# Kernel optimization log

Hardware: AMD Instinct MI355X
Metric: run time of the kernel (lower is better)

## Reference

```python
import jax, jax.numpy as jnp
import numpy as np
import math

B, S, E = 2, 2048, 1024
H, D = 16, 64
LAMBDA_INIT = 0.8
GN_EPS = 1e-5


def setup_inputs() -> dict:
    key = jax.random.key(0)
    ks = jax.random.split(key, 12)
    s = 0.02
    inputs = jax.random.normal(ks[0], (B, S, E), jnp.float32)
    attention_mask = jnp.ones((B, S), jnp.float32)
    token_indices = jnp.sort(jax.random.randint(ks[1], (B, S), 0, S), axis=-1)
    Wq = jax.random.normal(ks[2], (2 * H * D, E), jnp.float32) * s
    Wk = jax.random.normal(ks[3], (2 * H * D, E), jnp.float32) * s
    Wv = jax.random.normal(ks[4], (H * D, E), jnp.float32) * s
    Wo = jax.random.normal(ks[5], (E, H * D), jnp.float32) * s
    lam_q1 = jax.random.normal(ks[6], (D,), jnp.float32) * 0.1
    lam_q2 = jax.random.normal(ks[7], (D,), jnp.float32) * 0.1
    lam_k1 = jax.random.normal(ks[8], (D,), jnp.float32) * 0.1
    lam_k2 = jax.random.normal(ks[9], (D,), jnp.float32) * 0.1
    gn_w = jnp.ones((H * D,), jnp.float32)
    gn_b = jnp.zeros((H * D,), jnp.float32)
    return dict(inputs=inputs, attention_mask=attention_mask, token_indices=token_indices,
                Wq=Wq, Wk=Wk, Wv=Wv, Wo=Wo,
                lam_q1=lam_q1, lam_q2=lam_q2, lam_k1=lam_k1, lam_k2=lam_k2,
                gn_w=gn_w, gn_b=gn_b)


def reference(inputs, attention_mask, token_indices, Wq, Wk, Wv, Wo,
              lam_q1, lam_q2, lam_k1, lam_k2, gn_w, gn_b):
    b, s, e = inputs.shape
    # projections: q,k have doubled head dim (differential), v is standard
    q = (inputs @ Wq.T).reshape(b, s, H, 2 * D).transpose(0, 2, 1, 3)  # [B,H,S,2D]
    k = (inputs @ Wk.T).reshape(b, s, H, 2 * D).transpose(0, 2, 1, 3)
    v = (inputs @ Wv.T).reshape(b, s, H, D).transpose(0, 2, 1, 3)      # [B,H,S,D]
    Q1, Q2 = q[..., :D], q[..., D:]
    K1, K2 = k[..., :D], k[..., D:]
    scale = 1.0 / math.sqrt(D)
    s1 = jnp.einsum('bhqd,bhkd->bhqk', Q1, K1) * scale
    s2 = jnp.einsum('bhqd,bhkd->bhqk', Q2, K2) * scale
    # ALiBi bias: slopes[h] * (pos_q - pos_k), subtracted
    slopes = 2.0 ** (-8.0 * jnp.arange(1, H + 1, dtype=jnp.float32) / H)
    pos = token_indices.astype(jnp.float32)                            # [B,S]
    pos_diff = pos[:, :, None] - pos[:, None, :]                       # [B,S,S]
    bias = slopes[None, :, None, None] * pos_diff[:, None, :, :]       # [B,H,S,S]
    # causal + padding masks
    causal = jnp.triu(jnp.full((s, s), -1e9, jnp.float32), 1)[None, None]
    pad = (1.0 - attention_mask)[:, None, None, :] * -1e9
    s1 = s1 - bias + causal + pad
    s2 = s2 - bias + causal + pad
    w1 = jax.nn.softmax(s1, axis=-1)
    w2 = jax.nn.softmax(s2, axis=-1)
    lam = jnp.exp(jnp.dot(lam_q1, lam_k1)) - jnp.exp(jnp.dot(lam_q2, lam_k2)) + LAMBDA_INIT
    w = w1 - lam * w2
    out = jnp.einsum('bhqk,bhkd->bhqd', w, v)                          # [B,H,S,D]
    # GroupNorm(num_groups=H, num_channels=H*D) over channels-first layout [B,C,S]
    x = out.transpose(0, 2, 1, 3).reshape(b, s, H * D).transpose(0, 2, 1)  # [B,C,S]
    xg = x.reshape(b, H, D * s)
    mean = xg.mean(axis=-1, keepdims=True)
    var = xg.var(axis=-1, keepdims=True)
    xn = ((xg - mean) / jnp.sqrt(var + GN_EPS)).reshape(b, H * D, s)
    xn = xn * gn_w[None, :, None] + gn_b[None, :, None]
    xn = xn * (1.0 - LAMBDA_INIT)
    attn = xn.transpose(0, 2, 1)                                       # [B,S,H*D]
    return attn @ Wo.T
```

## Files before the change

kernel.cpp:

```cpp
#include <hip/hip_runtime.h>
#include <hip/hip_bf16.h>

typedef __hip_bfloat16 bf16;
typedef float f32x4 __attribute__((ext_vector_type(4)));
typedef float fvec4 __attribute__((ext_vector_type(4)));
typedef short s16x8 __attribute__((ext_vector_type(8)));

#define NB_B 2
#define NB_S 2048
#define NB_E 1024
#define NB_H 16
#define NB_D 64

typedef const __attribute__((address_space(1))) void* GPTR;
typedef __attribute__((address_space(3))) void* LPTR;

__device__ __forceinline__ void gld16(const void* g, void* l) {
  __builtin_amdgcn_global_load_lds((GPTR)g, (LPTR)l, 16, 0, 0);
}

__device__ __forceinline__ s16x8 ld8(const bf16* p) { return *(const s16x8*)p; }

__device__ __forceinline__ f32x4 MFMA(s16x8 a, s16x8 b, f32x4 c) {
  return __builtin_amdgcn_mfma_f32_16x16x32_bf16(a, b, c, 0, 0, 0);
}

struct __align__(8) bf16x4 { bf16 a, b, c, d; };

__global__ void prep_kernel(const float* __restrict__ inputs,
                            const float* __restrict__ wq, const float* __restrict__ wk,
                            const float* __restrict__ wv, const float* __restrict__ wo,
                            const float* __restrict__ lq1, const float* __restrict__ lq2,
                            const float* __restrict__ lk1, const float* __restrict__ lk2,
                            bf16* __restrict__ xbf,
                            bf16* __restrict__ oq, bf16* __restrict__ ok,
                            bf16* __restrict__ ov, bf16* __restrict__ oo,
                            float* __restrict__ lamo) {
  const int blk = blockIdx.x;
  if (blk < 4096) {
    int i = blk * 256 + threadIdx.x;
    fvec4 v = ((const fvec4*)inputs)[i];
    bf16x4 o = { bf16(v.x), bf16(v.y), bf16(v.z), bf16(v.w) };
    ((bf16x4*)xbf)[i] = o;
  } else if (blk < 10240) {
    int i = (blk - 4096) * 256 + threadIdx.x;
    const float* src; bf16* dst; int off;
    if (i < 524288)       { src = wq; dst = oq; off = i; }
    else if (i < 1048576) { src = wk; dst = ok; off = i - 524288; }
    else if (i < 1310720) { src = wv; dst = ov; off = i - 1048576; }
    else                  { src = wo; dst = oo; off = i - 1310720; }
    fvec4 v = ((const fvec4*)src)[off];
    bf16x4 o = { bf16(v.x), bf16(v.y), bf16(v.z), bf16(v.w) };
    ((bf16x4*)dst)[off] = o;
  } else {
    int l = threadIdx.x;
    if (l < 64) {
      float d1 = lq1[l] * lk1[l];
      float d2 = lq2[l] * lk2[l];
#pragma unroll
      for (int o = 32; o; o >>= 1) { d1 += __shfl_xor(d1, o); d2 += __shfl_xor(d2, o); }
      if (l == 0) lamo[0] = expf(d1) - expf(d2) + 0.8f;
    }
  }
}

__global__ void combo_kernel(const int* __restrict__ tok, const float* __restrict__ amask,
                             float* __restrict__ combo) {
  int i = blockIdx.x * 256 + threadIdx.x;
  int hh = i >> 12, bs = i & 4095;
  float slopeL = exp2f(-0.5f * (float)(hh + 1)) * 1.44269504088896340736f;
  combo[i] = slopeL * (float)tok[bs] + (amask[bs] - 1.f) * 1.44269504e9f;
}

__global__ void gn_coef(const float* __restrict__ gnp, const float* __restrict__ gw,
                        const float* __restrict__ gb,
                        float* __restrict__ Sc, float* __restrict__ Tc) {
  int i = blockIdx.x * 256 + threadIdx.x;
  int b = i >> 10, c = i & 1023;
  int bh = b * 16 + (c >> 6);
  float mean = gnp[bh * 2] * (1.f / 131072.f);
  float var = gnp[bh * 2 + 1] * (1.f / 131072.f) - mean * mean;
  float rstd = rsqrtf(var + 1e-5f) * 0.2f;
  float S = rstd * gw[c];
  Sc[i] = S;
  Tc[i] = 0.2f * gb[c] - mean * S;
}

template <int EPI>
__global__ __launch_bounds__(256) void gemm_bt(const bf16* __restrict__ A,
                                               const bf16* __restrict__ Bw,
                                               bf16* __restrict__ Ob,
                                               bf16* __restrict__ Ob2,
                                               bf16* __restrict__ Ob3,
                                               float* __restrict__ Of,
                                               int Kd, float oscale) {
  __shared__ bf16 As[2][128 * 32];
  __shared__ bf16 Bs[2][128 * 32];
  const int tid = threadIdx.x;
  const int lane = tid & 63;
  const int fr = lane & 15, fq = lane >> 4;
  const int wave = tid >> 6;
  const int wr = (wave >> 1) * 64, wc = (wave & 1) * 64;
  const size_t m0 = (size_t)blockIdx.x * 128, n0 = (size_t)blockIdx.y * 128;

  f32x4 acc[4][4];
#pragma unroll
  for (int i = 0; i < 4; i++)
#pragma unroll
    for (int j = 0; j < 4; j++) acc[i][j] = f32x4{0.f, 0.f, 0.f, 0.f};

  const int ca = tid, cb = tid + 256;
  const bf16* ga0 = A + (m0 + (ca >> 2)) * Kd + (ca & 3) * 8;
  const bf16* ga1 = A + (m0 + (cb >> 2)) * Kd + (cb & 3) * 8;
  const bf16* gb0 = Bw + (n0 + (ca >> 2)) * Kd + (ca & 3) * 8;
  const bf16* gb1 = Bw + (n0 + (cb >> 2)) * Kd + (cb & 3) * 8;

  gld16(ga0, &As[0][ca * 8]);
  gld16(ga1, &As[0][cb * 8]);
  gld16(gb0, &Bs[0][ca * 8]);
  gld16(gb1, &Bs[0][cb * 8]);
  __syncthreads();

  const int NKT = Kd >> 5;
  for (int kti = 0; kti < NKT; ++kti) {
    const int cur = kti & 1;
    if (kti + 1 < NKT) {
      const int kt = (kti + 1) << 5;
      gld16(ga0 + kt, &As[cur ^ 1][ca * 8]);
      gld16(ga1 + kt, &As[cur ^ 1][cb * 8]);
      gld16(gb0 + kt, &Bs[cur ^ 1][ca * 8]);
      gld16(gb1 + kt, &Bs[cur ^ 1][cb * 8]);
    }
    s16x8 af[4], bfv[4];
#pragma unroll
    for (int mi = 0; mi < 4; mi++) af[mi] = ld8(&As[cur][(wr + mi * 16 + fr) * 32 + fq * 8]);
#pragma unroll
    for (int ni = 0; ni < 4; ni++) bfv[ni] = ld8(&Bs[cur][(wc + ni * 16 + fr) * 32 + fq * 8]);
#pragma unroll
    for (int mi = 0; mi < 4; mi++)
#pragma unroll
      for (int ni = 0; ni < 4; ni++)
        acc[mi][ni] = MFMA(af[mi], bfv[ni], acc[mi][ni]);
    __syncthreads();
  }

  bf16* dst = Ob;
  size_t nsub = 0;
  float osc = oscale;
  bool isV = false;
  if constexpr (EPI == 0) {
    if (n0 >= 4096)      { dst = Ob3; nsub = 4096; osc = 1.0f; isV = true; }
    else if (n0 >= 2048) { dst = Ob2; nsub = 2048; osc = 1.0f; }
  }

  if constexpr (EPI == 0) {
    if (isV) {
#pragma unroll
      for (int mi = 0; mi < 4; mi++)
#pragma unroll
        for (int ni = 0; ni < 4; ni++) {
          size_t m = m0 + wr + mi * 16 + fq * 4;
          size_t n = n0 + wc + ni * 16 + fr;
          size_t nn = n - 4096;
          size_t b = m >> 11, s = m & 2047, h = nn >> 6, d = nn & 63;
          bf16x4 o = { bf16(acc[mi][ni][0]), bf16(acc[mi][ni][1]),
                       bf16(acc[mi][ni][2]), bf16(acc[mi][ni][3]) };
          *(bf16x4*)&dst[((b * NB_H + h) * NB_D + d) * NB_S + s] = o;
        }
    } else {
#pragma unroll
      for (int mi = 0; mi < 4; mi++)
#pragma unroll
        for (int ni = 0; ni < 4; ni++)
#pragma unroll
          for (int i = 0; i < 4; i++) {
            size_t m = m0 + wr + mi * 16 + fq * 4 + i;
            size_t n = n0 + wc + ni * 16 + fr;
            float v = acc[mi][ni][i] * osc;
            size_t nn = n - nsub;
            size_t b = m >> 11, s = m & 2047, h = nn >> 7, dd = nn & 127;
            dst[((b * NB_H + h) * NB_S + s) * 128 + dd] = bf16(v);
          }
    }
  } else {
#pragma unroll
    for (int mi = 0; mi < 4; mi++)
#pragma unroll
      for (int ni = 0; ni < 4; ni++)
#pragma unroll
        for (int i = 0; i < 4; i++) {
          size_t m = m0 + wr + mi * 16 + fq * 4 + i;
          size_t n = n0 + wc + ni * 16 + fr;
          Of[m * 1024 + n] = acc[mi][ni][i] * oscale;
        }
  }
}

__device__ __forceinline__ s16x8 gn_chunk(const bf16* __restrict__ Xb, size_t base, int tb,
                                          int k, const float* __restrict__ Sc,
                                          const float* __restrict__ Tc) {
  s16x8 xv = *(const s16x8*)(Xb + base + (size_t)(k >> 6) * 131072 + (k & 63));
  const float* sp = Sc + tb + k;
  const float* tp = Tc + tb + k;
  fvec4 s0v = *(const fvec4*)sp, s1v = *(const fvec4*)(sp + 4);
  fvec4 t0v = *(const fvec4*)tp, t1v = *(const fvec4*)(tp + 4);
  float sv[8] = { s0v.x, s0v.y, s0v.z, s0v.w, s1v.x, s1v.y, s1v.z, s1v.w };
  float tv[8] = { t0v.x, t0v.y, t0v.z, t0v.w, t1v.x, t1v.y, t1v.z, t1v.w };
  bf16 o8[8];
#pragma unroll
  for (int j = 0; j < 8; j++) {
    const float xf = __uint_as_float(((unsigned)(unsigned short)xv[j]) << 16);
    o8[j] = bf16(xf * sv[j] + tv[j]);
  }
  return *(const s16x8*)o8;
}

__global__ __launch_bounds__(256) void gemm_out(const bf16* __restrict__ Xb,
                                                const bf16* __restrict__ Bw,
                                                const float* __restrict__ Sc,
                                                const float* __restrict__ Tc,
                                                float* __restrict__ Of) {
  __shared__ bf16 As[2][128 * 32];
  __shared__ bf16 Bs[2][128 * 32];
  const int tid = threadIdx.x;
  const int lane = tid & 63;
  const int fr = lane & 15, fq = lane >> 4;
  const int wave = tid >> 6;
  const int wr = (wave >> 1) * 64, wc = (wave & 1) * 64;
  const size_t m0 = (size_t)blockIdx.x * 128, n0 = (size_t)blockIdx.y * 128;

  f32x4 acc[4][4];
#pragma unroll
  for (int i = 0; i < 4; i++)
#pragma unroll
    for (int j = 0; j < 4; j++) acc[i][j] = f32x4{0.f, 0.f, 0.f, 0.f};

  const int ca = tid, cb = tid + 256;
  const int ma = (int)m0 + (ca >> 2), mb = (int)m0 + (cb >> 2);
  const int koa = (ca & 3) * 8, kob = (cb & 3) * 8;
  const size_t basea = (size_t)(ma >> 11) * 2097152 + (size_t)(ma & 2047) * 64;
  const size_t baseb = (size_t)(mb >> 11) * 2097152 + (size_t)(mb & 2047) * 64;
  const int tba = (ma >> 11) * 1024, tbb = (mb >> 11) * 1024;

  const bf16* gb0 = Bw + (n0 + (ca >> 2)) * 1024 + koa;
  const bf16* gb1 = Bw + (n0 + (cb >> 2)) * 1024 + kob;

  {
    s16x8 a0 = gn_chunk(Xb, basea, tba, koa, Sc, Tc);
    s16x8 a1 = gn_chunk(Xb, baseb, tbb, kob, Sc, Tc);
    gld16(gb0, &Bs[0][ca * 8]);
    gld16(gb1, &Bs[0][cb * 8]);
    *(s16x8*)&As[0][ca * 8] = a0;
    *(s16x8*)&As[0][cb * 8] = a1;
  }
  __syncthreads();

  for (int kti = 0; kti < 32; ++kti) {
    const int cur = kti & 1;
    s16x8 na0, na1;
    if (kti + 1 < 32) {
      const int kt = (kti + 1) << 5;
      na0 = gn_chunk(Xb, basea, tba, kt + koa, Sc, Tc);
      na1 = gn_chunk(Xb, baseb, tbb, kt + kob, Sc, Tc);
      gld16(gb0 + kt, &Bs[cur ^ 1][ca * 8]);
      gld16(gb1 + kt, &Bs[cur ^ 1][cb * 8]);
    }
    s16x8 af[4], bfv[4];
#pragma unroll
    for (int mi = 0; mi < 4; mi++) af[mi] = ld8(&As[cur][(wr + mi * 16 + fr) * 32 + fq * 8]);
#pragma unroll
    for (int ni = 0; ni < 4; ni++) bfv[ni] = ld8(&Bs[cur][(wc + ni * 16 + fr) * 32 + fq * 8]);
#pragma unroll
    for (int mi = 0; mi < 4; mi++)
#pragma unroll
      for (int ni = 0; ni < 4; ni++)
        acc[mi][ni] = MFMA(af[mi], bfv[ni], acc[mi][ni]);
    if (kti + 1 < 32) {
      *(s16x8*)&As[cur ^ 1][ca * 8] = na0;
      *(s16x8*)&As[cur ^ 1][cb * 8] = na1;
    }
    __syncthreads();
  }

#pragma unroll
  for (int mi = 0; mi < 4; mi++)
#pragma unroll
    for (int ni = 0; ni < 4; ni++)
#pragma unroll
      for (int i = 0; i < 4; i++) {
        size_t m = m0 + wr + mi * 16 + fq * 4 + i;
        size_t n = n0 + wc + ni * 16 + fr;
        Of[m * 1024 + n] = acc[mi][ni][i];
      }
}

__global__ __launch_bounds__(512, 2) void attn_kernel(
    const bf16* __restrict__ Q, const bf16* __restrict__ Kk, const bf16* __restrict__ Vt,
    const float* __restrict__ combo,
    const float* __restrict__ lamp, bf16* __restrict__ Xb, float* __restrict__ gnp) {
  __shared__ bf16 Ks[2][2][4096];
  __shared__ bf16 Vs[2][4096];
  __shared__ bf16 Ps[8][1024];
  __shared__ float gs[8][2];

  const int tid = threadIdx.x, lane = tid & 63, wave = tid >> 6;
  const int fr = lane & 15, fq = lane >> 4;
  const int id = blockIdx.x;
  const int w = id >> 3;
  const int bh = (id & 7) * 4 + (w & 3);
  const int qj = 15 - (w >> 2);
  const int b = bh >> 4, h = bh & 15;

  const float lam = lamp[0];
  const float* comboH = combo + ((size_t)h * NB_B + b) * NB_S;

  const bf16* Kbase = Kk + (size_t)bh * NB_S * 128;
  const bf16* Vbase = Vt + (size_t)bh * NB_D * NB_S;

  const s16x8 onesv = { 0x3F80, 0x3F80, 0x3F80, 0x3F80, 0x3F80, 0x3F80, 0x3F80, 0x3F80 };

  int adr[4][2], pw[4], pr[2];
#pragma unroll
  for (int nt = 0; nt < 4; nt++) {
    const int r = nt * 16 + fr;
#pragma unroll
    for (int kk = 0; kk < 2; kk++) adr[nt][kk] = r * 64 + (((kk * 4 + fq) ^ (r & 7)) << 3);
    pw[nt] = fr * 64 + (((nt * 4 + fq) ^ ((fr & 7) << 1)) << 2);
  }
  pr[0] = fr * 64 + (((fq * 2) ^ ((fr & 7) << 1)) << 2);
  pr[1] = fr * 64 + (((8 + fq * 2) ^ ((fr & 7) << 1)) << 2);

  const bf16* gK[2]; int lK[2];
#pragma unroll
  for (int i = 0; i < 2; i++) {
    int c = tid + i * 512, set = c >> 9, cc = c & 511;
    int row = cc >> 3, col8 = cc & 7, sc = col8 ^ (row & 7);
    gK[i] = Kbase + (size_t)row * 128 + set * 64 + sc * 8;
    lK[i] = set * 4096 + cc * 8;
  }
  const bf16* gV; int lV;
  {
    int c = tid;
    int row = c >> 3, col8 = c & 7, sc = col8 ^ (row & 7);
    gV = Vbase + (size_t)row * NB_S + sc * 8;
    lV = c * 8;
  }

  const int q0 = qj * 128;
  const int qw = q0 + wave * 16;
  const int ntiles = 2 * qj + 2;

  const bf16* qrow = Q + ((size_t)bh * NB_S + qw + fr) * 128;
  s16x8 q1[2], q2[2];
  q1[0] = ld8(qrow + fq * 8);       q1[1] = ld8(qrow + 32 + fq * 8);
  q2[0] = ld8(qrow + 64 + fq * 8);  q2[1] = ld8(qrow + 96 + fq * 8);

  const int qg = qw + fr;

  float m1 = -1e30f, m2 = -1e30f;
  f32x4 acc1[4], acc2[4];
  f32x4 accL1 = f32x4{0.f,0.f,0.f,0.f}, accL2 = f32x4{0.f,0.f,0.f,0.f};
#pragma unroll
  for (int nt = 0; nt < 4; nt++) { acc1[nt] = f32x4{0.f,0.f,0.f,0.f}; acc2[nt] = f32x4{0.f,0.f,0.f,0.f}; }

#pragma unroll
  for (int i = 0; i < 2; i++) gld16(gK[i], &Ks[0][0][0] + lK[i]);
  gld16(gV, &Vs[0][0] + lV);
  fvec4 cmb[4];
#pragma unroll
  for (int nt = 0; nt < 4; nt++) cmb[nt] = *(const fvec4*)(comboH + nt * 16 + fq * 4);
  __syncthreads();

  for (int t = 0; t < ntiles; ++t) {
    const int cur = t & 1;
    const int kv0 = t * 64;
    if (t + 1 < ntiles) {
#pragma unroll
      for (int i = 0; i < 2; i++)
        gld16(gK[i] + (size_t)(kv0 + 64) * 128, &Ks[cur ^ 1][0][0] + lK[i]);
      gld16(gV + (size_t)(kv0 + 64), &Vs[cur ^ 1][0] + lV);
    }

    const bool active = (kv0 <= qw + 15);
    if (active) {
      const bf16* kb0 = &Ks[cur][0][0];
      const bf16* kb1 = &Ks[cur][1][0];

      f32x4 c1[4], c2[4];
      __builtin_amdgcn_s_setprio(1);
#pragma unroll
      for (int nt = 0; nt < 4; nt++) {
        c1[nt] = MFMA(ld8(kb0 + adr[nt][0]), q1[0], cmb[nt]);
        c2[nt] = MFMA(ld8(kb1 + adr[nt][0]), q2[0], cmb[nt]);
      }
      {
        const float* cp = comboH + (t + 1 < ntiles ? kv0 + 64 : kv0);
#pragma unroll
        for (int nt = 0; nt < 4; nt++) cmb[nt] = *(const fvec4*)(cp + nt * 16 + fq * 4);
      }
#pragma unroll
      for (int nt = 0; nt < 4; nt++) {
        c1[nt] = MFMA(ld8(kb0 + adr[nt][1]), q1[1], c1[nt]);
        c2[nt] = MFMA(ld8(kb1 + adr[nt][1]), q2[1], c2[nt]);
      }
      __builtin_amdgcn_s_setprio(0);

      if (kv0 + 63 > qw) {
#pragma unroll
        for (int nt = 0; nt < 4; nt++)
#pragma unroll
          for (int i = 0; i < 4; i++)
            if (kv0 + nt * 16 + fq * 4 + i > qg) { c1[nt][i] = -1e30f; c2[nt][i] = -1e30f; }
      }

      s16x8 vf[4][2];
#pragma unroll
      for (int nt = 0; nt < 4; nt++)
#pragma unroll
        for (int kk = 0; kk < 2; kk++)
          vf[nt][kk] = ld8(&Vs[cur][adr[nt][kk]]);

      {
        float pm = fmaxf(fmaxf(fmaxf(c1[0][0], c1[0][1]), fmaxf(c1[0][2], c1[0][3])),
                         fmaxf(fmaxf(c1[1][0], c1[1][1]), fmaxf(c1[1][2], c1[1][3])));
        pm = fmaxf(pm, fmaxf(fmaxf(fmaxf(c1[2][0], c1[2][1]), fmaxf(c1[2][2], c1[2][3])),
                             fmaxf(fmaxf(c1[3][0], c1[3][1]), fmaxf(c1[3][2], c1[3][3]))));
        pm = fmaxf(pm, __shfl_xor(pm, 16));
        pm = fmaxf(pm, __shfl_xor(pm, 32));
        if (__any(pm > m1 + 8.f)) {
          const float nm = fmaxf(m1, pm);
          const float cor = exp2f(m1 - nm);
          m1 = nm;
#pragma unroll
          for (int i = 0; i < 4; i++) {
            const float ci = __shfl(cor, fq * 4 + i);
            accL1[i] *= ci;
#pragma unroll
            for (int nt = 0; nt < 4; nt++) acc1[nt][i] *= ci;
          }
        }
#pragma unroll
        for (int nt = 0; nt < 4; nt++) {
          bf16x4 pk = { bf16(exp2f(c1[nt][0] - m1)), bf16(exp2f(c1[nt][1] - m1)),
                        bf16(exp2f(c1[nt][2] - m1)), bf16(exp2f(c1[nt][3] - m1)) };
          *(bf16x4*)&Ps[wave][pw[nt]] = pk;
        }
        __builtin_amdgcn_s_setprio(1);
#pragma unroll
        for (int kk = 0; kk < 2; kk++) {
          const s16x8 pa = ld8(&Ps[wave][pr[kk]]);
          accL1 = MFMA(pa, onesv, accL1);
#pragma unroll
          for (int nt = 0; nt < 4; nt++) acc1[nt] = MFMA(pa, vf[nt][kk], acc1[nt]);
        }
        __builtin_amdgcn_s_setprio(0);
      }
      {
        float pm = fmaxf(fmaxf(fmaxf(c2[0][0], c2[0][1]), fmaxf(c2[0][2], c2[0][3])),
                         fmaxf(fmaxf(c2[1][0], c2[1][1]), fmaxf(c2[1][2], c2[1][3])));
        pm = fmaxf(pm, fmaxf(fmaxf(fmaxf(c2[2][0], c2[2][1]), fmaxf(c2[2][2], c2[2][3])),
                             fmaxf(fmaxf(c2[3][0], c2[3][1]), fmaxf(c2[3][2], c2[3][3]))));
        pm = fmaxf(pm, __shfl_xor(pm, 16));
        pm = fmaxf(pm, __shfl_xor(pm, 32));
        if (__any(pm > m2 + 8.f)) {
          const float nm = fmaxf(m2, pm);
          const float cor = exp2f(m2 - nm);
          m2 = nm;
#pragma unroll
          for (int i = 0; i < 4; i++) {
            const float ci = __shfl(cor, fq * 4 + i);
            accL2[i] *= ci;
#pragma unroll
            for (int nt = 0; nt < 4; nt++) acc2[nt][i] *= ci;
          }
        }
#pragma unroll
        for (int nt = 0; nt < 4; nt++) {
          bf16x4 pk = { bf16(exp2f(c2[nt][0] - m2)), bf16(exp2f(c2[nt][1] - m2)),
                        bf16(exp2f(c2[nt][2] - m2)), bf16(exp2f(c2[nt][3] - m2)) };
          *(bf16x4*)&Ps[wave][pw[nt]] = pk;
        }
        __builtin_amdgcn_s_setprio(1);
#pragma unroll
        for (int kk = 0; kk < 2; kk++) {
          const s16x8 pa = ld8(&Ps[wave][pr[kk]]);
          accL2 = MFMA(pa, onesv, accL2);
#pragma unroll
          for (int nt = 0; nt < 4; nt++) acc2[nt] = MFMA(pa, vf[nt][kk], acc2[nt]);
        }
        __builtin_amdgcn_s_setprio(0);
      }
    }

    __syncthreads();
  }

  float r1b[4], r2b[4];
#pragma unroll
  for (int i = 0; i < 4; i++) { r1b[i] = 1.f / accL1[i]; r2b[i] = lam / accL2[i]; }
  float s = 0.f, s2 = 0.f;
#pragma unroll
  for (int nt = 0; nt < 4; nt++)
#pragma unroll
    for (int i = 0; i < 4; i++) {
      const float v = acc1[nt][i] * r1b[i] - acc2[nt][i] * r2b[i];
      Xb[((size_t)bh * NB_S + qw + fq * 4 + i) * NB_D + nt * 16 + fr] = bf16(v);
      s += v; s2 += v * v;
    }
#pragma unroll
  for (int o = 32; o; o >>= 1) { s += __shfl_xor(s, o); s2 += __shfl_xor(s2, o); }
  if (lane == 0) { gs[wave][0] = s; gs[wave][1] = s2; }
  __syncthreads();
  if (tid == 0) {
    float S = 0.f, S2 = 0.f;
#pragma unroll
    for (int i = 0; i < 8; i++) { S += gs[i][0]; S2 += gs[i][1]; }
    atomicAdd(&gnp[bh * 2], S);
    atomicAdd(&gnp[bh * 2 + 1], S2);
  }
}

extern "C" void kernel_launch(void* const* d_in, const int* in_sizes, int n_in,
                              void* d_out, int out_size, void* d_ws, size_t ws_size,
                              hipStream_t stream) {
  const float* inputs = (const float*)d_in[0];
  const float* amask  = (const float*)d_in[1];
  const int*   tok    = (const int*)d_in[2];
  const float* Wq = (const float*)d_in[3];
  const float* Wk = (const float*)d_in[4];
  const float* Wv = (const float*)d_in[5];
  const float* Wo = (const float*)d_in[6];
  const float* lq1 = (const float*)d_in[7];
  const float* lq2 = (const float*)d_in[8];
  const float* lk1 = (const float*)d_in[9];
  const float* lk2 = (const float*)d_in[10];
  const float* gw = (const float*)d_in[11];
  const float* gb = (const float*)d_in[12];
  float* out = (float*)d_out;
  char* ws = (char*)d_ws;

  bf16* Xbf = (bf16*)(ws + 0);
  bf16* Wqb = (bf16*)(ws + 8388608);
  bf16* Wkb = (bf16*)(ws + 12582912);
  bf16* Wvb = (bf16*)(ws + 16777216);
  bf16* Xb  = (bf16*)(ws + 0);
  float* combo = (float*)(ws + 16777216);
  bf16* Qb  = (bf16*)(ws + 18874368);
  bf16* Kb  = (bf16*)(ws + 35651584);
  bf16* Vtb = (bf16*)(ws + 52428800);
  bf16* Wob = (bf16*)(ws + 60817408);
  float* lam = (float*)(ws + 62914560);
  float* gnp = (float*)(ws + 62914816);
  float* Sc  = (float*)(ws + 62915584);
  float* Tc  = (float*)(ws + 62923776);

  const float QSCALE = 0.125f * 1.44269504088896340736f;

  (void)hipMemsetAsync(gnp, 0, 512, stream);
  prep_kernel<<<10241, 256, 0, stream>>>(inputs, Wq, Wk, Wv, Wo, lq1, lq2, lk1, lk2,
                                         Xbf, Wqb, Wkb, Wvb, Wob, lam);

  gemm_bt<0><<<dim3(32, 40), 256, 0, stream>>>(Xbf, Wqb, Qb, Kb, Vtb, nullptr, 1024, QSCALE);

  combo_kernel<<<256, 256, 0, stream>>>(tok, amask, combo);

  attn_kernel<<<512, 512, 0, stream>>>(Qb, Kb, Vtb, combo, lam, Xb, gnp);

  gn_coef<<<8, 256, 0, stream>>>(gnp, gw, gb, Sc, Tc);

  gemm_out<<<dim3(32, 8), 256, 0, stream>>>(Xb, Wob, Sc, Tc, out);
}
```

Measured before the change: 212.3 us.

## Fold GroupNorm scale into per-batch Wo and bias into output offset

The GroupNorm affine (per-batch, per-channel scale and shift) is moved from the A operand of the output GEMM into a per-batch scaled copy of Wo plus a per-batch output bias vector, both computed by a new gnfix kernel. The output GEMM can then stream X through direct global-to-LDS loads instead of register-side normalization and conversion in its main loop. In exchange it adds a 4 MB weight-scaling pass and a row-reduction of 2048 dot products of length 1024, plus a slightly different bf16 rounding point.

```diff
diff --git a/kernel.cpp b/kernel.cpp
--- a/kernel.cpp
+++ b/kernel.cpp
@@ -23,6 +23,10 @@
 
 __device__ __forceinline__ f32x4 MFMA(s16x8 a, s16x8 b, f32x4 c) {
   return __builtin_amdgcn_mfma_f32_16x16x32_bf16(a, b, c, 0, 0, 0);
+}
+
+__device__ __forceinline__ float b2f(short u) {
+  return __uint_as_float(((unsigned)(unsigned short)u) << 16);
 }
 
 struct __align__(8) bf16x4 { bf16 a, b, c, d; };
@@ -72,18 +76,45 @@
   combo[i] = slopeL * (float)tok[bs] + (amask[bs] - 1.f) * 1.44269504e9f;
 }
 
-__global__ void gn_coef(const float* __restrict__ gnp, const float* __restrict__ gw,
-                        const float* __restrict__ gb,
-                        float* __restrict__ Sc, float* __restrict__ Tc) {
-  int i = blockIdx.x * 256 + threadIdx.x;
-  int b = i >> 10, c = i & 1023;
-  int bh = b * 16 + (c >> 6);
-  float mean = gnp[bh * 2] * (1.f / 131072.f);
-  float var = gnp[bh * 2 + 1] * (1.f / 131072.f) - mean * mean;
-  float rstd = rsqrtf(var + 1e-5f) * 0.2f;
-  float S = rstd * gw[c];
-  Sc[i] = S;
-  Tc[i] = 0.2f * gb[c] - mean * S;
+__global__ void gnfix(const float* __restrict__ gnp, const float* __restrict__ gw,
+                      const float* __restrict__ gb, const bf16* __restrict__ Wob,
+                      bf16* __restrict__ Wos, float* __restrict__ Tout) {
+  const int blk = blockIdx.x;
+  if (blk < 1024) {
+    int i = blk * 256 + threadIdx.x;
+    int b = i >> 17, rem = i & 131071;
+    int n = rem >> 7, c = (rem & 127) * 8;
+    int bh = b * 16 + (c >> 6);
+    float mean = gnp[bh * 2] * (1.f / 131072.f);
+    float var = gnp[bh * 2 + 1] * (1.f / 131072.f) - mean * mean;
+    float r = rsqrtf(var + 1e-5f) * 0.2f;
+    s16x8 wv = *(const s16x8*)(Wob + n * 1024 + c);
+    fvec4 g0 = *(const fvec4*)(gw + c), g1 = *(const fvec4*)(gw + c + 4);
+    float gv[8] = { g0.x, g0.y, g0.z, g0.w, g1.x, g1.y, g1.z, g1.w };
+    bf16 o8[8];
+#pragma unroll
+    for (int j = 0; j < 8; j++) o8[j] = bf16(b2f(wv[j]) * r * gv[j]);
+    *(s16x8*)(Wos + (size_t)b * 1048576 + n * 1024 + c) = *(const s16x8*)o8;
+  } else {
+    int g = (blk - 1024) * 256 + threadIdx.x;
+    int b = g >> 10, n = g & 1023;
+    float acc = 0.f;
+    for (int c = 0; c < 1024; c += 8) {
+      int bh = b * 16 + (c >> 6);
+      float mean = gnp[bh * 2] * (1.f / 131072.f);
+      float var = gnp[bh * 2 + 1] * (1.f / 131072.f) - mean * mean;
+      float r = rsqrtf(var + 1e-5f) * 0.2f;
+      s16x8 wv = *(const s16x8*)(Wob + n * 1024 + c);
+      fvec4 g0 = *(const fvec4*)(gw + c), g1 = *(const fvec4*)(gw + c + 4);
+      fvec4 bb0 = *(const fvec4*)(gb + c), bb1 = *(const fvec4*)(gb + c + 4);
+      float gv[8] = { g0.x, g0.y, g0.z, g0.w, g1.x, g1.y, g1.z, g1.w };
+      float bv[8] = { bb0.x, bb0.y, bb0.z, bb0.w, bb1.x, bb1.y, bb1.z, bb1.w };
+#pragma unroll
+      for (int j = 0; j < 8; j++)
+        acc += (0.2f * bv[j] - mean * r * gv[j]) * b2f(wv[j]);
+    }
+    Tout[g] = acc;
+  }
 }
 
 template <int EPI>
@@ -196,29 +227,9 @@
   }
 }
 
-__device__ __forceinline__ s16x8 gn_chunk(const bf16* __restrict__ Xb, size_t base, int tb,
-                                          int k, const float* __restrict__ Sc,
-                                          const float* __restrict__ Tc) {
-  s16x8 xv = *(const s16x8*)(Xb + base + (size_t)(k >> 6) * 131072 + (k & 63));
-  const float* sp = Sc + tb + k;
-  const float* tp = Tc + tb + k;
-  fvec4 s0v = *(const fvec4*)sp, s1v = *(const fvec4*)(sp + 4);
-  fvec4 t0v = *(const fvec4*)tp, t1v = *(const fvec4*)(tp + 4);
-  float sv[8] = { s0v.x, s0v.y, s0v.z, s0v.w, s1v.x, s1v.y, s1v.z, s1v.w };
-  float tv[8] = { t0v.x, t0v.y, t0v.z, t0v.w, t1v.x, t1v.y, t1v.z, t1v.w };
-  bf16 o8[8];
-#pragma unroll
-  for (int j = 0; j < 8; j++) {
-    const float xf = __uint_as_float(((unsigned)(unsigned short)xv[j]) << 16);
-    o8[j] = bf16(xf * sv[j] + tv[j]);
-  }
-  return *(const s16x8*)o8;
-}
-
 __global__ __launch_bounds__(256) void gemm_out(const bf16* __restrict__ Xb,
-                                                const bf16* __restrict__ Bw,
-                                                const float* __restrict__ Sc,
-                                                const float* __restrict__ Tc,
+                                                const bf16* __restrict__ Wos,
+                                                const float* __restrict__ Tout,
                                                 float* __restrict__ Of) {
   __shared__ bf16 As[2][128 * 32];
   __shared__ bf16 Bs[2][128 * 32];
@@ -228,6 +239,7 @@
   const int wave = tid >> 6;
   const int wr = (wave >> 1) * 64, wc = (wave & 1) * 64;
   const size_t m0 = (size_t)blockIdx.x * 128, n0 = (size_t)blockIdx.y * 128;
+  const int bb = (int)(m0 >> 11);
 
   f32x4 acc[4][4];
 #pragma unroll
@@ -236,32 +248,26 @@
     for (int j = 0; j < 4; j++) acc[i][j] = f32x4{0.f, 0.f, 0.f, 0.f};
 
   const int ca = tid, cb = tid + 256;
-  const int ma = (int)m0 + (ca >> 2), mb = (int)m0 + (cb >> 2);
-  const int koa = (ca & 3) * 8, kob = (cb & 3) * 8;
-  const size_t basea = (size_t)(ma >> 11) * 2097152 + (size_t)(ma & 2047) * 64;
-  const size_t baseb = (size_t)(mb >> 11) * 2097152 + (size_t)(mb & 2047) * 64;
-  const int tba = (ma >> 11) * 1024, tbb = (mb >> 11) * 1024;
-
-  const bf16* gb0 = Bw + (n0 + (ca >> 2)) * 1024 + koa;
-  const bf16* gb1 = Bw + (n0 + (cb >> 2)) * 1024 + kob;
-
-  {
-    s16x8 a0 = gn_chunk(Xb, basea, tba, koa, Sc, Tc);
-    s16x8 a1 = gn_chunk(Xb, baseb, tbb, kob, Sc, Tc);
-    gld16(gb0, &Bs[0][ca * 8]);
-    gld16(gb1, &Bs[0][cb * 8]);
-    *(s16x8*)&As[0][ca * 8] = a0;
-    *(s16x8*)&As[0][cb * 8] = a1;
-  }
+  const int s0 = (int)(m0 & 2047);
+  const bf16* pa0 = Xb + (size_t)bb * 2097152 + (size_t)(s0 + (ca >> 2)) * 64 + (ca & 3) * 8;
+  const bf16* pa1 = Xb + (size_t)bb * 2097152 + (size_t)(s0 + (cb >> 2)) * 64 + (cb & 3) * 8;
+  const bf16* Bw = Wos + (size_t)bb * 1048576;
+  const bf16* gb0 = Bw + (n0 + (ca >> 2)) * 1024 + (ca & 3) * 8;
+  const bf16* gb1 = Bw + (n0 + (cb >> 2)) * 1024 + (cb & 3) * 8;
+
+  gld16(pa0, &As[0][ca * 8]);
+  gld16(pa1, &As[0][cb * 8]);
+  gld16(gb0, &Bs[0][ca * 8]);
+  gld16(gb1, &Bs[0][cb * 8]);
   __syncthreads();
 
   for (int kti = 0; kti < 32; ++kti) {
     const int cur = kti & 1;
-    s16x8 na0, na1;
     if (kti + 1 < 32) {
       const int kt = (kti + 1) << 5;
-      na0 = gn_chunk(Xb, basea, tba, kt + koa, Sc, Tc);
-      na1 = gn_chunk(Xb, baseb, tbb, kt + kob, Sc, Tc);
+      const size_t aoff = (size_t)(kt >> 6) * 131072 + (kt & 63);
+      gld16(pa0 + aoff, &As[cur ^ 1][ca * 8]);
+      gld16(pa1 + aoff, &As[cur ^ 1][cb * 8]);
       gld16(gb0 + kt, &Bs[cur ^ 1][ca * 8]);
       gld16(gb1 + kt, &Bs[cur ^ 1][cb * 8]);
     }
@@ -275,13 +281,12 @@
 #pragma unroll
       for (int ni = 0; ni < 4; ni++)
         acc[mi][ni] = MFMA(af[mi], bfv[ni], acc[mi][ni]);
-    if (kti + 1 < 32) {
-      *(s16x8*)&As[cur ^ 1][ca * 8] = na0;
-      *(s16x8*)&As[cur ^ 1][cb * 8] = na1;
-    }
     __syncthreads();
   }
 
+  float tv[4];
+#pragma unroll
+  for (int ni = 0; ni < 4; ni++) tv[ni] = Tout[bb * 1024 + n0 + wc + ni * 16 + fr];
 #pragma unroll
   for (int mi = 0; mi < 4; mi++)
 #pragma unroll
@@ -290,7 +295,7 @@
       for (int i = 0; i < 4; i++) {
         size_t m = m0 + wr + mi * 16 + fq * 4 + i;
         size_t n = n0 + wc + ni * 16 + fr;
-        Of[m * 1024 + n] = acc[mi][ni][i];
+        Of[m * 1024 + n] = acc[mi][ni][i] + tv[ni];
       }
 }
 
@@ -546,13 +551,13 @@
   bf16* Xb  = (bf16*)(ws + 0);
   float* combo = (float*)(ws + 16777216);
   bf16* Qb  = (bf16*)(ws + 18874368);
+  bf16* Wos = (bf16*)(ws + 18874368);
   bf16* Kb  = (bf16*)(ws + 35651584);
   bf16* Vtb = (bf16*)(ws + 52428800);
   bf16* Wob = (bf16*)(ws + 60817408);
   float* lam = (float*)(ws + 62914560);
   float* gnp = (float*)(ws + 62914816);
-  float* Sc  = (float*)(ws + 62915584);
-  float* Tc  = (float*)(ws + 62923776);
+  float* Tout = (float*)(ws + 62915584);
 
   const float QSCALE = 0.125f * 1.44269504088896340736f;
 
@@ -566,7 +571,7 @@
 
   attn_kernel<<<512, 512, 0, stream>>>(Qb, Kb, Vtb, combo, lam, Xb, gnp);
 
-  gn_coef<<<8, 256, 0, stream>>>(gnp, gw, gb, Sc, Tc);
-
-  gemm_out<<<dim3(32, 8), 256, 0, stream>>>(Xb, Wob, Sc, Tc, out);
-}
+  gnfix<<<1032, 256, 0, stream>>>(gnp, gw, gb, Wob, Wos, Tout);
+
+  gemm_out<<<dim3(32, 8), 256, 0, stream>>>(Xb, Wos, Tout, out);
+}
```

New measurement: 236.4 us. 11.3% more time.
